# Performance work log

Hardware: AMD Instinct MI355X
Metric: run time of the kernel (lower is better)

Reference implementation:

```python
import jax, jax.numpy as jnp
import numpy as np

B, T, C = 4, 2048, 768
N_HEAD = 12
HS = C // N_HEAD

def setup_inputs() -> dict:
    key = jax.random.key(0)
    ks = jax.random.split(key, 5)
    s = 0.02
    return {
        "x": jax.random.normal(ks[0], (B, T, C), dtype=jnp.float32),
        "w_attn": jax.random.normal(ks[1], (C, 3 * C), dtype=jnp.float32) * s,
        "b_attn": jnp.zeros((3 * C,), dtype=jnp.float32),
        "w_proj": jax.random.normal(ks[2], (C, C), dtype=jnp.float32) * s,
        "b_proj": jnp.zeros((C,), dtype=jnp.float32),
    }

def reference(x, w_attn, b_attn, w_proj, b_proj):
    Bx, Tx, Cx = x.shape
    qkv = x @ w_attn + b_attn                      # [B,T,3C]
    q, k, v = jnp.split(qkv, 3, axis=-1)
    # [B,H,T,hs]
    q = q.reshape(Bx, Tx, N_HEAD, HS).transpose(0, 2, 1, 3)
    k = k.reshape(Bx, Tx, N_HEAD, HS).transpose(0, 2, 1, 3)
    v = v.reshape(Bx, Tx, N_HEAD, HS).transpose(0, 2, 1, 3)
    att = jnp.einsum('bhqd,bhkd->bhqk', q, k) * (1.0 / jnp.sqrt(jnp.float32(HS)))
    mask = jnp.tril(jnp.ones((Tx, Tx), dtype=bool))  # causal
    att = jnp.where(mask, att, jnp.float32(-jnp.inf))
    att = jax.nn.softmax(att, axis=-1)
    y = jnp.einsum('bhqk,bhkd->bhqd', att, v)
    y = y.transpose(0, 2, 1, 3).reshape(Bx, Tx, Cx)
    return y @ w_proj + b_proj
```

## Files before the change

### kernel.cpp

```cpp
#include <hip/hip_runtime.h>

#define BB 4
#define TT 2048
#define CC 768
#define QKVW 2304
#define NHH 12
#define HSS 64
#define NQT64 (TT / 64)

typedef __attribute__((ext_vector_type(4))) float floatx4;
typedef __attribute__((ext_vector_type(8))) short shortx8;
typedef __attribute__((ext_vector_type(4))) short shortx4;

__device__ __forceinline__ unsigned short f2bf(float f) {
  union { float f; unsigned int u; } cv; cv.f = f;
  unsigned int u = cv.u;
  u += 0x7FFFu + ((u >> 16) & 1u);
  return (unsigned short)(u >> 16);
}
__device__ __forceinline__ unsigned short bfp(float f) {
  union { float f; unsigned int u; } cv; cv.f = f;
  return (unsigned short)((cv.u + 0x8000u) >> 16);
}

__device__ __forceinline__ void async_copy16(const void* g, void* l) {
  __builtin_amdgcn_global_load_lds(
      (const __attribute__((address_space(1))) unsigned int*)g,
      (__attribute__((address_space(3))) unsigned int*)l, 16, 0, 0);
}

__device__ __forceinline__ floatx4 mfma16(shortx4 a, shortx4 b, floatx4 c) {
  return __builtin_amdgcn_mfma_f32_16x16x16bf16_1k(a, b, c, 0, 0, 0);
}

__global__ void convert_x(const float* __restrict__ x, unsigned short* __restrict__ xb, int n4) {
  int i = blockIdx.x * blockDim.x + threadIdx.x;
  const int stride = gridDim.x * blockDim.x;
  for (; i < n4; i += stride) {
    float4 v = ((const float4*)x)[i];
    shortx4 s;
    s.x = (short)f2bf(v.x); s.y = (short)f2bf(v.y);
    s.z = (short)f2bf(v.z); s.w = (short)f2bf(v.w);
    ((shortx4*)xb)[i] = s;
  }
}

__global__ __launch_bounds__(256)
void transpose_w(const float* __restrict__ w, unsigned short* __restrict__ wt, int K, int N) {
  __shared__ short tile[64 * 68];
  const int n0 = blockIdx.x * 64, k0 = blockIdx.y * 64;
  const int tid = threadIdx.x;
  {
    const int tr = tid >> 4, tc = (tid & 15) * 4;
#pragma unroll
    for (int i = 0; i < 4; ++i) {
      float4 v = *(const float4*)(w + (size_t)(k0 + tr + 16 * i) * N + n0 + tc);
      short* d = &tile[(tr + 16 * i) * 68 + tc];
      d[0] = (short)f2bf(v.x); d[1] = (short)f2bf(v.y);
      d[2] = (short)f2bf(v.z); d[3] = (short)f2bf(v.w);
    }
  }
  __syncthreads();
  {
    const int wr = tid >> 3, wc = (tid & 7) * 8;
#pragma unroll
    for (int j = 0; j < 2; ++j) {
      const int n = wr + 32 * j;
      shortx8 s;
#pragma unroll
      for (int e = 0; e < 8; ++e) s[e] = tile[(wc + e) * 68 + n];
      *(shortx8*)(wt + (size_t)(n0 + n) * K + k0 + wc) = s;
    }
  }
}

__global__ __launch_bounds__(256)
void transpose_v(const unsigned short* __restrict__ qkv, unsigned short* __restrict__ Vt) {
  __shared__ short tile[64 * 72];
  const int t0 = blockIdx.x * 64;
  const int bh = blockIdx.y;
  const int b = bh / NHH, h = bh % NHH;
  const int tid = threadIdx.x;
  {
    const int tr = tid >> 3, tc = (tid & 7) * 8;
#pragma unroll
    for (int i = 0; i < 2; ++i) {
      shortx8 v = *(const shortx8*)(qkv + ((size_t)(b * TT + t0 + tr + 32 * i)) * QKVW + 2 * CC + h * HSS + tc);
      *(shortx8*)&tile[(tr + 32 * i) * 72 + tc] = v;
    }
  }
  __syncthreads();
  {
    const int dr = tid >> 3, tc = (tid & 7) * 8;
#pragma unroll
    for (int j = 0; j < 2; ++j) {
      const int d = dr + 32 * j;
      shortx8 s;
#pragma unroll
      for (int e = 0; e < 8; ++e) s[e] = tile[(tc + e) * 72 + d];
      *(shortx8*)(Vt + ((size_t)bh * HSS + d) * TT + t0 + tc) = s;
    }
  }
}

template<bool OUT_BF16, bool QSCALE>
__global__ __launch_bounds__(256)
void gemm_tn(const unsigned short* __restrict__ A, const unsigned short* __restrict__ Bt,
             const float* __restrict__ bias, void* __restrict__ Cp, int M, int N, int K) {
  __shared__ short As[128 * 32];
  __shared__ short Bs[128 * 32];
  const int tid = threadIdx.x, lane = tid & 63, wave = tid >> 6;
  const int row = lane & 15, quad = lane >> 4;
  const int wm = (wave >> 1) * 64, wn = (wave & 1) * 64;
  const int m0 = blockIdx.x * 128, n0 = blockIdx.y * 128;

  floatx4 acc[4][4] = {};

  const int sr = wave * 32 + (lane >> 2);
  const int sc = (lane & 3) * 8;
  const unsigned short* aP = A + (size_t)(m0 + sr) * K + sc;
  const unsigned short* bP = Bt + (size_t)(n0 + sr) * K + sc;
  short* asBase = &As[(wave * 32) * 32];
  short* bsBase = &Bs[(wave * 32) * 32];

  for (int k0 = 0; k0 < K; k0 += 32) {
#pragma unroll
    for (int i = 0; i < 2; ++i) {
      async_copy16(aP + (size_t)(16 * i) * K + k0, asBase + i * 512);
      async_copy16(bP + (size_t)(16 * i) * K + k0, bsBase + i * 512);
    }
    __syncthreads();
    shortx8 af[4], bf[4];
#pragma unroll
    for (int g = 0; g < 4; ++g) {
      af[g] = *(const shortx8*)&As[(wm + g * 16 + row) * 32 + quad * 8];
      bf[g] = *(const shortx8*)&Bs[(wn + g * 16 + row) * 32 + quad * 8];
    }
#pragma unroll
    for (int mg = 0; mg < 4; ++mg)
#pragma unroll
      for (int ng = 0; ng < 4; ++ng)
        acc[mg][ng] = __builtin_amdgcn_mfma_f32_16x16x32_bf16(af[mg], bf[ng], acc[mg][ng], 0, 0, 0);
    __syncthreads();
  }

#pragma unroll
  for (int mg = 0; mg < 4; ++mg) {
    const int m = m0 + wm + mg * 16 + quad * 4;
#pragma unroll
    for (int ng = 0; ng < 4; ++ng) {
      const int n = n0 + wn + ng * 16 + row;
      const float bv = bias[n];
      const float scl = (QSCALE && n < CC) ? 0.180336881f : 1.0f;
#pragma unroll
      for (int r = 0; r < 4; ++r) {
        const float val = (acc[mg][ng][r] + bv) * scl;
        if (OUT_BF16) ((unsigned short*)Cp)[(size_t)(m + r) * N + n] = f2bf(val);
        else          ((float*)Cp)[(size_t)(m + r) * N + n] = val;
      }
    }
  }
}

__global__ __launch_bounds__(256)
void attn_kernel(const unsigned short* __restrict__ qkv, const unsigned short* __restrict__ Vt,
                 unsigned short* __restrict__ y) {
  constexpr int STR = 72;
  __shared__ short Kd[2][64 * STR];
  __shared__ short Vd[2][64 * STR];

  const int p = blockIdx.x;
  const int h = blockIdx.y, b = blockIdx.z;
  const int bh = b * NHH + h;
  const int tid = threadIdx.x, lane = tid & 63, wave = tid >> 6;
  const int row = lane & 15, quad = lane >> 4;

  const int srow = tid >> 3;
  const int scol = (tid & 7) * 8;
  const unsigned short* kSrc = qkv + ((size_t)(b * TT)) * QKVW + CC + h * HSS;
  const unsigned short* vSrc = Vt + ((size_t)bh * HSS) * TT;

  for (int item = 0; item < 2; ++item) {
    const int qt = item == 0 ? (NQT64 - 1 - p) : p;
    const int qbase = qt * 64 + wave * 16;

    shortx8 qf0, qf1;
    {
      const unsigned short* qp = qkv + ((size_t)(b * TT) + qbase + row) * QKVW + h * HSS;
      qf0 = *(const shortx8*)(qp + quad * 8);
      qf1 = *(const shortx8*)(qp + 32 + quad * 8);
    }

    float l_acc = 0.0f;
    floatx4 o[4];
#pragma unroll
    for (int dg = 0; dg < 4; ++dg) o[dg] = (floatx4)(0.0f);

    shortx8 kr[2], vr[2];
#pragma unroll
    for (int i = 0; i < 2; ++i) {
      kr[i] = *(const shortx8*)(kSrc + (size_t)(srow + 32 * i) * QKVW + scol);
      vr[i] = *(const shortx8*)(vSrc + (size_t)(srow + 32 * i) * TT + scol);
    }
#pragma unroll
    for (int i = 0; i < 2; ++i) {
      *(shortx8*)&Kd[0][(srow + 32 * i) * STR + scol] = kr[i];
      *(shortx8*)&Vd[0][(srow + 32 * i) * STR + scol] = vr[i];
    }
    __syncthreads();

    const int nk = qt + 1;
    for (int kt = 0; kt < nk; ++kt) {
      const int cur = kt & 1;
      if (kt + 1 < nk) {
#pragma unroll
        for (int i = 0; i < 2; ++i) {
          kr[i] = *(const shortx8*)(kSrc + (size_t)((kt + 1) * 64 + srow + 32 * i) * QKVW + scol);
          vr[i] = *(const shortx8*)(vSrc + (size_t)(srow + 32 * i) * TT + (kt + 1) * 64 + scol);
        }
      }
      {
        const short* Kc = &Kd[cur][0];
        const short* Vc = &Vd[cur][0];
        floatx4 sa[4];
#pragma unroll
        for (int mg = 0; mg < 4; ++mg) {
          shortx8 kf0 = *(const shortx8*)&Kc[(mg * 16 + row) * STR + quad * 8];
          shortx8 kf1 = *(const shortx8*)&Kc[(mg * 16 + row) * STR + 32 + quad * 8];
          floatx4 t = __builtin_amdgcn_mfma_f32_16x16x32_bf16(kf0, qf0, (floatx4)(0.0f), 0, 0, 0);
          sa[mg] = __builtin_amdgcn_mfma_f32_16x16x32_bf16(kf1, qf1, t, 0, 0, 0);
        }
        if (kt == qt) {
#pragma unroll
          for (int mg = 0; mg < 4; ++mg) {
            const int kg = kt * 64 + mg * 16 + quad * 4;
#pragma unroll
            for (int r = 0; r < 4; ++r)
              if (kg + r > qbase + row) sa[mg][r] = -1e30f;
          }
        }
        shortx4 pfr[4];
#pragma unroll
        for (int mg = 0; mg < 4; ++mg) {
          shortx4 pk;
#pragma unroll
          for (int r = 0; r < 4; ++r) {
            const float pe = __builtin_amdgcn_exp2f(sa[mg][r]);
            l_acc += pe;
            pk[r] = (short)bfp(pe);
          }
          pfr[mg] = pk;
        }
#pragma unroll
        for (int dg = 0; dg < 4; ++dg) {
#pragma unroll
          for (int mg = 0; mg < 4; ++mg) {
            shortx4 vf = *(const shortx4*)&Vc[(dg * 16 + row) * STR + mg * 16 + quad * 4];
            o[dg] = mfma16(pfr[mg], vf, o[dg]);
          }
        }
      }
      if (kt + 1 < nk) {
        const int nb = (kt + 1) & 1;
#pragma unroll
        for (int i = 0; i < 2; ++i) {
          *(shortx8*)&Kd[nb][(srow + 32 * i) * STR + scol] = kr[i];
          *(shortx8*)&Vd[nb][(srow + 32 * i) * STR + scol] = vr[i];
        }
      }
      __syncthreads();
    }

    {
      float l = l_acc;
      l += __shfl_xor(l, 16);
      l += __shfl_xor(l, 32);
      const float linv = 1.0f / l;
#pragma unroll
      for (int r = 0; r < 4; ++r) {
        const float lo = __shfl(linv, quad * 4 + r);
        unsigned short* yp = y + ((size_t)(b * TT) + qbase + quad * 4 + r) * CC + h * HSS;
#pragma unroll
        for (int dg = 0; dg < 4; ++dg)
          yp[dg * 16 + row] = bfp(o[dg][r] * lo);
      }
    }
  }
}

extern "C" void kernel_launch(void* const* d_in, const int* in_sizes, int n_in,
                              void* d_out, int out_size, void* d_ws, size_t ws_size,
                              hipStream_t stream) {
  const float* x      = (const float*)d_in[0];
  const float* w_attn = (const float*)d_in[1];
  const float* b_attn = (const float*)d_in[2];
  const float* w_proj = (const float*)d_in[3];
  const float* b_proj = (const float*)d_in[4];
  float* out = (float*)d_out;

  char* ws = (char*)d_ws;
  unsigned short* xb  = (unsigned short*)ws;
  unsigned short* y   = (unsigned short*)ws;
  unsigned short* qkv = (unsigned short*)(ws + 12582912);
  unsigned short* wta = (unsigned short*)(ws + 50331648);
  unsigned short* Vt  = (unsigned short*)(ws + 50331648);
  unsigned short* wtp = (unsigned short*)(ws + 62914560);

  const int M = BB * TT;

  convert_x<<<1024, 256, 0, stream>>>(x, xb, (M * CC) / 4);
  transpose_w<<<dim3(QKVW / 64, CC / 64), 256, 0, stream>>>(w_attn, wta, CC, QKVW);
  transpose_w<<<dim3(CC / 64, CC / 64), 256, 0, stream>>>(w_proj, wtp, CC, CC);

  gemm_tn<true, true><<<dim3(M / 128, QKVW / 128), 256, 0, stream>>>(
      xb, wta, b_attn, (void*)qkv, M, QKVW, CC);

  transpose_v<<<dim3(TT / 64, BB * NHH), 256, 0, stream>>>(qkv, Vt);

  attn_kernel<<<dim3(NQT64 / 2, NHH, BB), 256, 0, stream>>>(qkv, Vt, y);

  gemm_tn<false, false><<<dim3(M / 128, CC / 128), 256, 0, stream>>>(
      y, wtp, b_proj, (void*)out, M, CC, CC);
}
```

Measured before the change: 235.9 us.

## Double K-step in GEMM and compute softmax row sums with MFMA

```diff
diff --git a/kernel.cpp b/kernel.cpp
--- a/kernel.cpp
+++ b/kernel.cpp
@@ -21,6 +21,10 @@
 __device__ __forceinline__ unsigned short bfp(float f) {
   union { float f; unsigned int u; } cv; cv.f = f;
   return (unsigned short)((cv.u + 0x8000u) >> 16);
+}
+__device__ __forceinline__ unsigned short bft(float f) {
+  union { float f; unsigned int u; } cv; cv.f = f;
+  return (unsigned short)(cv.u >> 16);
 }
 
 __device__ __forceinline__ void async_copy16(const void* g, void* l) {
@@ -107,8 +111,8 @@
 __global__ __launch_bounds__(256)
 void gemm_tn(const unsigned short* __restrict__ A, const unsigned short* __restrict__ Bt,
              const float* __restrict__ bias, void* __restrict__ Cp, int M, int N, int K) {
-  __shared__ short As[128 * 32];
-  __shared__ short Bs[128 * 32];
+  __shared__ short As0[128 * 32], As1[128 * 32];
+  __shared__ short Bs0[128 * 32], Bs1[128 * 32];
   const int tid = threadIdx.x, lane = tid & 63, wave = tid >> 6;
   const int row = lane & 15, quad = lane >> 4;
   const int wm = (wave >> 1) * 64, wn = (wave & 1) * 64;
@@ -120,27 +124,43 @@
   const int sc = (lane & 3) * 8;
   const unsigned short* aP = A + (size_t)(m0 + sr) * K + sc;
   const unsigned short* bP = Bt + (size_t)(n0 + sr) * K + sc;
-  short* asBase = &As[(wave * 32) * 32];
-  short* bsBase = &Bs[(wave * 32) * 32];
-
-  for (int k0 = 0; k0 < K; k0 += 32) {
+  short* as0Base = &As0[(wave * 32) * 32];
+  short* as1Base = &As1[(wave * 32) * 32];
+  short* bs0Base = &Bs0[(wave * 32) * 32];
+  short* bs1Base = &Bs1[(wave * 32) * 32];
+
+  for (int k0 = 0; k0 < K; k0 += 64) {
 #pragma unroll
     for (int i = 0; i < 2; ++i) {
-      async_copy16(aP + (size_t)(16 * i) * K + k0, asBase + i * 512);
-      async_copy16(bP + (size_t)(16 * i) * K + k0, bsBase + i * 512);
+      async_copy16(aP + (size_t)(16 * i) * K + k0,      as0Base + i * 512);
+      async_copy16(aP + (size_t)(16 * i) * K + k0 + 32, as1Base + i * 512);
+      async_copy16(bP + (size_t)(16 * i) * K + k0,      bs0Base + i * 512);
+      async_copy16(bP + (size_t)(16 * i) * K + k0 + 32, bs1Base + i * 512);
     }
     __syncthreads();
-    shortx8 af[4], bf[4];
-#pragma unroll
-    for (int g = 0; g < 4; ++g) {
-      af[g] = *(const shortx8*)&As[(wm + g * 16 + row) * 32 + quad * 8];
-      bf[g] = *(const shortx8*)&Bs[(wn + g * 16 + row) * 32 + quad * 8];
-    }
-#pragma unroll
-    for (int mg = 0; mg < 4; ++mg)
-#pragma unroll
-      for (int ng = 0; ng < 4; ++ng)
-        acc[mg][ng] = __builtin_amdgcn_mfma_f32_16x16x32_bf16(af[mg], bf[ng], acc[mg][ng], 0, 0, 0);
+    {
+      shortx8 af[4], bf[4];
+#pragma unroll
+      for (int g = 0; g < 4; ++g) {
+        af[g] = *(const shortx8*)&As0[(wm + g * 16 + row) * 32 + quad * 8];
+        bf[g] = *(const shortx8*)&Bs0[(wn + g * 16 + row) * 32 + quad * 8];
+      }
+#pragma unroll
+      for (int mg = 0; mg < 4; ++mg)
+#pragma unroll
+        for (int ng = 0; ng < 4; ++ng)
+          acc[mg][ng] = __builtin_amdgcn_mfma_f32_16x16x32_bf16(af[mg], bf[ng], acc[mg][ng], 0, 0, 0);
+#pragma unroll
+      for (int g = 0; g < 4; ++g) {
+        af[g] = *(const shortx8*)&As1[(wm + g * 16 + row) * 32 + quad * 8];
+        bf[g] = *(const shortx8*)&Bs1[(wn + g * 16 + row) * 32 + quad * 8];
+      }
+#pragma unroll
+      for (int mg = 0; mg < 4; ++mg)
+#pragma unroll
+        for (int ng = 0; ng < 4; ++ng)
+          acc[mg][ng] = __builtin_amdgcn_mfma_f32_16x16x32_bf16(af[mg], bf[ng], acc[mg][ng], 0, 0, 0);
+    }
     __syncthreads();
   }
 
@@ -180,6 +200,8 @@
   const unsigned short* kSrc = qkv + ((size_t)(b * TT)) * QKVW + CC + h * HSS;
   const unsigned short* vSrc = Vt + ((size_t)bh * HSS) * TT;
 
+  const shortx4 ones = {(short)0x3F80, (short)0x3F80, (short)0x3F80, (short)0x3F80};
+
   for (int item = 0; item < 2; ++item) {
     const int qt = item == 0 ? (NQT64 - 1 - p) : p;
     const int qbase = qt * 64 + wave * 16;
@@ -191,7 +213,7 @@
       qf1 = *(const shortx8*)(qp + 32 + quad * 8);
     }
 
-    float l_acc = 0.0f;
+    floatx4 lf = (floatx4)(0.0f);
     floatx4 o[4];
 #pragma unroll
     for (int dg = 0; dg < 4; ++dg) o[dg] = (floatx4)(0.0f);
@@ -244,17 +266,15 @@
         for (int mg = 0; mg < 4; ++mg) {
           shortx4 pk;
 #pragma unroll
-          for (int r = 0; r < 4; ++r) {
-            const float pe = __builtin_amdgcn_exp2f(sa[mg][r]);
-            l_acc += pe;
-            pk[r] = (short)bfp(pe);
-          }
+          for (int r = 0; r < 4; ++r)
+            pk[r] = (short)bft(__builtin_amdgcn_exp2f(sa[mg][r]));
           pfr[mg] = pk;
         }
 #pragma unroll
-        for (int dg = 0; dg < 4; ++dg) {
-#pragma unroll
-          for (int mg = 0; mg < 4; ++mg) {
+        for (int mg = 0; mg < 4; ++mg) {
+          lf = mfma16(pfr[mg], ones, lf);
+#pragma unroll
+          for (int dg = 0; dg < 4; ++dg) {
             shortx4 vf = *(const shortx4*)&Vc[(dg * 16 + row) * STR + mg * 16 + quad * 4];
             o[dg] = mfma16(pfr[mg], vf, o[dg]);
           }
@@ -272,13 +292,9 @@
     }
 
     {
-      float l = l_acc;
-      l += __shfl_xor(l, 16);
-      l += __shfl_xor(l, 32);
-      const float linv = 1.0f / l;
 #pragma unroll
       for (int r = 0; r < 4; ++r) {
-        const float lo = __shfl(linv, quad * 4 + r);
+        const float lo = 1.0f / lf[r];
         unsigned short* yp = y + ((size_t)(b * TT) + qbase + quad * 4 + r) * CC + h * HSS;
 #pragma unroll
         for (int dg = 0; dg < 4; ++dg)
```

After: 223.2 us. -5.4%, faster.
